# Kernel optimization log

Measured on AMD Instinct MI355X. Metric: run time of the kernel, lower is better.

The kernel has to match this reference:

```python
import jax, jax.numpy as jnp
import numpy as np

B, C, H, W = 32, 1024, 32, 32  # NOTE: code requires C == H*W (see bmm below)
C_HALF = C // 2


def setup_inputs() -> dict:
    key = jax.random.key(0)
    ks = jax.random.split(key, 7)
    s_in = 1.0 / np.sqrt(C)
    return {
        "x": jax.random.normal(ks[0], (B, C, H, W), dtype=jnp.float32),
        "Wq": jax.random.normal(ks[1], (C_HALF, C), dtype=jnp.float32) * s_in,
        "bq": jax.random.normal(ks[2], (C_HALF,), dtype=jnp.float32) * 0.01,
        "Wk": jax.random.normal(ks[3], (C_HALF, C), dtype=jnp.float32) * s_in,
        "bk": jax.random.normal(ks[4], (C_HALF,), dtype=jnp.float32) * 0.01,
        "Wv": jax.random.normal(ks[5], (C, C), dtype=jnp.float32) * s_in,
        "bv": jax.random.normal(ks[6], (C,), dtype=jnp.float32) * 0.01,
    }


def reference(x, Wq, bq, Wk, bk, Wv, bv):
    b, c, h, w = x.shape
    hw = h * w
    xf = x.reshape(b, c, hw)  # [B, C, HW]
    # 1x1 convs are per-pixel linear maps over channels
    q = jnp.einsum('oc,bcn->bno', Wq, xf) + bq            # [B, HW, C/2]  (permuted)
    k = jnp.einsum('oc,bcn->bon', Wk, xf) + bk[:, None]   # [B, C/2, HW]
    v = jnp.einsum('oc,bcn->bno', Wv, xf) + bv            # [B, HW, C]   (permuted)
    attn = jax.nn.softmax(jnp.einsum('bno,bom->bnm', q, k), axis=-1)  # [B, HW, HW]
    # torch: bmm(value [B,HW,C], attention^T [B,HW,HW]) -> requires C == HW
    out = jnp.einsum('bik,bjk->bij', v, attn)  # [B, HW(=C), HW]
    out = out.reshape(b, c, h, w)
    return out + x
```

## Files before the change

### kernel.cpp

```cpp
#include <hip/hip_runtime.h>

typedef _Float16 f16;
typedef _Float16 f16x8 __attribute__((ext_vector_type(8)));
typedef float f32x4 __attribute__((ext_vector_type(4)));

__device__ __forceinline__ void g2lds16(const void* g, void* l) {
    __builtin_amdgcn_global_load_lds(
        (const __attribute__((address_space(1))) void*)g,
        (__attribute__((address_space(3))) void*)l, 16, 0, 0);
}

__global__ __launch_bounds__(256)
void prep_w(const float* __restrict__ Wq, const float* __restrict__ bq,
            const float* __restrict__ Wk, const float* __restrict__ bk,
            const float* __restrict__ Wv, const float* __restrict__ bv,
            f16* __restrict__ Wall, float* __restrict__ ball)
{
    const int idx = blockIdx.x * 256 + threadIdx.x;
    const int o = idx >> 10;
    const int c = idx & 1023;
    float w;
    if (o < 512)        w = Wq[idx];
    else if (o < 1024)  w = Wk[idx - 512 * 1024];
    else                w = Wv[idx - 1024 * 1024];
    Wall[idx] = (f16)w;
    if (c == 0)
        ball[o] = (o < 512) ? bq[o] : (o < 1024) ? bk[o - 512] : bv[o - 1024];
}

__global__ __launch_bounds__(256)
void transpose_cast(const float* __restrict__ x, f16* __restrict__ xT)
{
    __shared__ float t[32][33];
    const int b  = blockIdx.z;
    const int c0 = blockIdx.y << 5;
    const int n0 = blockIdx.x << 5;
    const int tx = threadIdx.x & 31, ty = threadIdx.x >> 5;
    const float* xb = x + (unsigned long long)b * (1024ull * 1024ull);
#pragma unroll
    for (int i = 0; i < 32; i += 8)
        t[ty + i][tx] = xb[(unsigned long long)(c0 + ty + i) * 1024ull + (n0 + tx)];
    __syncthreads();
    f16* ob = xT + (unsigned long long)b * (1024ull * 1024ull);
#pragma unroll
    for (int i = 0; i < 32; i += 8)
        ob[(unsigned long long)(n0 + ty + i) * 1024ull + (c0 + tx)] = (f16)t[tx][ty + i];
}

template <int EPI, int LDA, int LDB, int K, int LDO,
          long long SA, long long SB, long long SO, int SWZ>
__global__ __launch_bounds__(256)
void gemm_nt(const f16* __restrict__ A, const f16* __restrict__ Bm,
             const float* __restrict__ bias,
             f16* __restrict__ Oh, float* __restrict__ Of,
             const float* __restrict__ Xres)
{
    __shared__ f16 As[2 * 128 * 32];
    __shared__ f16 Bs[2 * 128 * 32];

    const int tid  = threadIdx.x;
    const int wave = tid >> 6;
    const int lane = tid & 63;
    const int quad = lane >> 4;
    const int l16  = lane & 15;
    const int wr   = (wave >> 1) << 6;
    const int wc   = (wave & 1) << 6;

    int bm, bn;
    if (SWZ) {
        const int g = blockIdx.x >> 7;
        const int r = blockIdx.x & 127;
        bm = ((g << 3) | (r & 7)) << 7;
        bn = (r >> 3) << 7;
    } else {
        bm = blockIdx.x << 7;
        bn = blockIdx.y << 7;
    }
    const int bz = blockIdx.z;

    const f16* Ab = A  + (unsigned long long)bz * (unsigned long long)SA;
    const f16* Bb = Bm + (unsigned long long)bz * (unsigned long long)SB;

    const int srow = lane >> 2;
    const int scol = (lane & 3) << 3;

    f32x4 acc[4][4] = {};

    for (int k0 = 0; k0 < K; k0 += 64) {
        __syncthreads();
#pragma unroll
        for (int kk = 0; kk < 2; ++kk) {
#pragma unroll
            for (int t = 0; t < 2; ++t) {
                const int rbase = t * 64 + wave * 16;
                g2lds16(Ab + (unsigned long long)(bm + rbase + srow) * LDA + (k0 + kk * 32 + scol),
                        As + kk * 4096 + rbase * 32 + lane * 8);
                g2lds16(Bb + (unsigned long long)(bn + rbase + srow) * LDB + (k0 + kk * 32 + scol),
                        Bs + kk * 4096 + rbase * 32 + lane * 8);
            }
        }
        __syncthreads();

#pragma unroll
        for (int kk = 0; kk < 2; ++kk) {
            f16x8 af[4], bf[4];
#pragma unroll
            for (int i = 0; i < 4; ++i)
                af[i] = *(const f16x8*)(As + kk * 4096 + (wr + i * 16 + l16) * 32 + quad * 8);
#pragma unroll
            for (int i = 0; i < 4; ++i)
                bf[i] = *(const f16x8*)(Bs + kk * 4096 + (wc + i * 16 + l16) * 32 + quad * 8);

#pragma unroll
            for (int mi = 0; mi < 4; ++mi)
#pragma unroll
                for (int ni = 0; ni < 4; ++ni)
                    acc[mi][ni] = __builtin_amdgcn_mfma_f32_16x16x32_f16(
                        af[mi], bf[ni], acc[mi][ni], 0, 0, 0);
        }
    }

#pragma unroll
    for (int mi = 0; mi < 4; ++mi) {
#pragma unroll
        for (int v = 0; v < 4; ++v) {
            const int row = bm + wr + mi * 16 + quad * 4 + v;
#pragma unroll
            for (int ni = 0; ni < 4; ++ni) {
                const int col = bn + wc + ni * 16 + l16;
                float val = acc[mi][ni][v];
                if (EPI == 0) {
                    val += bias[col];
                    Oh[(unsigned long long)row * LDO + col] = (f16)val;
                } else if (EPI == 1) {
                    Of[(unsigned long long)bz * (unsigned long long)SO +
                       (unsigned long long)row * LDO + col] = val;
                } else {
                    const unsigned long long off =
                        (unsigned long long)bz * (unsigned long long)SO +
                        (unsigned long long)row * LDO + col;
                    Of[off] = val + Xres[off];
                }
            }
        }
    }
}

__global__ __launch_bounds__(256)
void softmax_rows(const float* __restrict__ S, f16* __restrict__ P)
{
    const unsigned long long row = blockIdx.x;
    const int tid = threadIdx.x;
    const float4 v = ((const float4*)(S + row * 1024ull))[tid];

    float m = fmaxf(fmaxf(v.x, v.y), fmaxf(v.z, v.w));
#pragma unroll
    for (int off = 32; off; off >>= 1)
        m = fmaxf(m, __shfl_xor(m, off, 64));

    __shared__ float redm[4], reds[4];
    const int wave = tid >> 6, lane = tid & 63;
    if (lane == 0) redm[wave] = m;
    __syncthreads();
    m = fmaxf(fmaxf(redm[0], redm[1]), fmaxf(redm[2], redm[3]));

    const float e0 = __expf(v.x - m), e1 = __expf(v.y - m);
    const float e2 = __expf(v.z - m), e3 = __expf(v.w - m);
    float sum = e0 + e1 + e2 + e3;
#pragma unroll
    for (int off = 32; off; off >>= 1)
        sum += __shfl_xor(sum, off, 64);
    if (lane == 0) reds[wave] = sum;
    __syncthreads();
    sum = reds[0] + reds[1] + reds[2] + reds[3];
    const float inv = 1.0f / sum;

    union { f16 h[4]; uint2 u; } pk;
    pk.h[0] = (f16)(e0 * inv); pk.h[1] = (f16)(e1 * inv);
    pk.h[2] = (f16)(e2 * inv); pk.h[3] = (f16)(e3 * inv);
    ((uint2*)(P + row * 1024ull))[tid] = pk.u;
}

extern "C" void kernel_launch(void* const* d_in, const int* in_sizes, int n_in,
                              void* d_out, int out_size, void* d_ws, size_t ws_size,
                              hipStream_t stream)
{
    const float* x  = (const float*)d_in[0];
    const float* Wq = (const float*)d_in[1];
    const float* bq = (const float*)d_in[2];
    const float* Wk = (const float*)d_in[3];
    const float* bk = (const float*)d_in[4];
    const float* Wv = (const float*)d_in[5];
    const float* bv = (const float*)d_in[6];
    float* out = (float*)d_out;

    f16*   xT   = (f16*)d_ws;
    f16*   Wall = xT + 32ull * 1024 * 1024;
    float* ball = (float*)(Wall + 2048ull * 1024);
    f16*   QKV  = (f16*)(ball + 2048);
    float* S    = (float*)(QKV + 64ull * 1024 * 1024);
    f16*   P    = (f16*)(S + 32ull * 1024 * 1024);

    prep_w<<<8192, 256, 0, stream>>>(Wq, bq, Wk, bk, Wv, bv, Wall, ball);
    transpose_cast<<<dim3(32, 32, 32), 256, 0, stream>>>(x, xT);

    gemm_nt<0, 1024, 1024, 1024, 2048, 0ll, 0ll, 0ll, 1>
        <<<dim3(4096, 1, 1), 256, 0, stream>>>(
        xT, Wall, ball, QKV, nullptr, nullptr);

    gemm_nt<1, 2048, 2048, 512, 1024, 1024ll * 2048, 1024ll * 2048, 1024ll * 1024, 0>
        <<<dim3(8, 8, 32), 256, 0, stream>>>(
        QKV, QKV + 512, nullptr, nullptr, S, nullptr);

    softmax_rows<<<32768, 256, 0, stream>>>(S, P);

    gemm_nt<2, 2048, 1024, 1024, 1024, 1024ll * 2048, 1024ll * 1024, 1024ll * 1024, 0>
        <<<dim3(8, 8, 32), 256, 0, stream>>>(
        QKV + 1024, P, nullptr, nullptr, out, x);
}
```

Before: 644.4 us.

## Switch GEMMs to 32x32x16 MFMA with XOR-swizzled LDS, XCD-aware tile mapping, vectorized transpose

The GEMM kernel now uses 32x32x16 MFMA instructions on a 2x2 accumulator tile per wave, and the LDS tile holds a single 64-wide K slab with XOR swizzling. This is meant to cut LDS bank conflicts and the number of LDS reads per MFMA. The QKV projection's block swizzle now groups tiles by XCD (blockIdx & 7) to improve L2 locality across chiplets. The transpose-cast kernel moves to 64x64 tiles with float4 loads and 8-wide f16 stores to widen memory transactions. The epilogue writes become strided per lane, and the new row mapping and swizzle carry correctness risk.

```diff
diff --git a/kernel.cpp b/kernel.cpp
--- a/kernel.cpp
+++ b/kernel.cpp
@@ -2,7 +2,7 @@
 
 typedef _Float16 f16;
 typedef _Float16 f16x8 __attribute__((ext_vector_type(8)));
-typedef float f32x4 __attribute__((ext_vector_type(4)));
+typedef float f32x16 __attribute__((ext_vector_type(16)));
 
 __device__ __forceinline__ void g2lds16(const void* g, void* l) {
     __builtin_amdgcn_global_load_lds(
@@ -31,20 +31,36 @@
 __global__ __launch_bounds__(256)
 void transpose_cast(const float* __restrict__ x, f16* __restrict__ xT)
 {
-    __shared__ float t[32][33];
+    __shared__ float t[64][65];
     const int b  = blockIdx.z;
-    const int c0 = blockIdx.y << 5;
-    const int n0 = blockIdx.x << 5;
-    const int tx = threadIdx.x & 31, ty = threadIdx.x >> 5;
+    const int c0 = blockIdx.y << 6;
+    const int n0 = blockIdx.x << 6;
+    const int tid = threadIdx.x;
     const float* xb = x + (unsigned long long)b * (1024ull * 1024ull);
-#pragma unroll
-    for (int i = 0; i < 32; i += 8)
-        t[ty + i][tx] = xb[(unsigned long long)(c0 + ty + i) * 1024ull + (n0 + tx)];
+
+    {
+        const int cl = tid >> 4;
+        const int n4 = (tid & 15) << 2;
+#pragma unroll
+        for (int i = 0; i < 64; i += 16) {
+            const float4 v = *(const float4*)(xb + (unsigned long long)(c0 + cl + i) * 1024ull + (n0 + n4));
+            t[cl + i][n4 + 0] = v.x; t[cl + i][n4 + 1] = v.y;
+            t[cl + i][n4 + 2] = v.z; t[cl + i][n4 + 3] = v.w;
+        }
+    }
     __syncthreads();
-    f16* ob = xT + (unsigned long long)b * (1024ull * 1024ull);
-#pragma unroll
-    for (int i = 0; i < 32; i += 8)
-        ob[(unsigned long long)(n0 + ty + i) * 1024ull + (c0 + tx)] = (f16)t[tx][ty + i];
+    {
+        f16* ob = xT + (unsigned long long)b * (1024ull * 1024ull);
+        const int nl = tid >> 3;
+        const int c8 = (tid & 7) << 3;
+#pragma unroll
+        for (int i = 0; i < 64; i += 32) {
+            f16x8 h;
+#pragma unroll
+            for (int j = 0; j < 8; ++j) h[j] = (f16)t[c8 + j][nl + i];
+            *(f16x8*)(ob + (unsigned long long)(n0 + nl + i) * 1024ull + (c0 + c8)) = h;
+        }
+    }
 }
 
 template <int EPI, int LDA, int LDB, int K, int LDO,
@@ -55,23 +71,28 @@
              f16* __restrict__ Oh, float* __restrict__ Of,
              const float* __restrict__ Xres)
 {
-    __shared__ f16 As[2 * 128 * 32];
-    __shared__ f16 Bs[2 * 128 * 32];
+    __shared__ f16 As[128 * 64];
+    __shared__ f16 Bs[128 * 64];
 
     const int tid  = threadIdx.x;
     const int wave = tid >> 6;
     const int lane = tid & 63;
-    const int quad = lane >> 4;
-    const int l16  = lane & 15;
+    const int l31  = lane & 31;
+    const int half = lane >> 5;
     const int wr   = (wave >> 1) << 6;
     const int wc   = (wave & 1) << 6;
 
     int bm, bn;
     if (SWZ) {
-        const int g = blockIdx.x >> 7;
-        const int r = blockIdx.x & 127;
-        bm = ((g << 3) | (r & 7)) << 7;
-        bn = (r >> 3) << 7;
+        const int xcd   = blockIdx.x & 7;
+        const int local = blockIdx.x >> 3;
+        const int stl   = local >> 6;
+        const int sub   = local & 63;
+        const int st    = stl * 8 + xcd;
+        const int bmg   = st >> 1;
+        const int bng   = st & 1;
+        bm = (bmg * 8 + (sub & 7)) << 7;
+        bn = (bng * 8 + (sub >> 3)) << 7;
     } else {
         bm = blockIdx.x << 7;
         bn = blockIdx.y << 7;
@@ -81,57 +102,56 @@
     const f16* Ab = A  + (unsigned long long)bz * (unsigned long long)SA;
     const f16* Bb = Bm + (unsigned long long)bz * (unsigned long long)SB;
 
-    const int srow = lane >> 2;
-    const int scol = (lane & 3) << 3;
-
-    f32x4 acc[4][4] = {};
+    const int srow = lane >> 3;
+    const int scol = (((lane & 7) ^ srow) << 3);
+
+    f32x16 acc[2][2] = {};
 
     for (int k0 = 0; k0 < K; k0 += 64) {
         __syncthreads();
 #pragma unroll
-        for (int kk = 0; kk < 2; ++kk) {
-#pragma unroll
-            for (int t = 0; t < 2; ++t) {
-                const int rbase = t * 64 + wave * 16;
-                g2lds16(Ab + (unsigned long long)(bm + rbase + srow) * LDA + (k0 + kk * 32 + scol),
-                        As + kk * 4096 + rbase * 32 + lane * 8);
-                g2lds16(Bb + (unsigned long long)(bn + rbase + srow) * LDB + (k0 + kk * 32 + scol),
-                        Bs + kk * 4096 + rbase * 32 + lane * 8);
+        for (int t = 0; t < 4; ++t) {
+            const int rb = t * 32 + wave * 8;
+            g2lds16(Ab + (unsigned long long)(bm + rb + srow) * LDA + (k0 + scol),
+                    As + rb * 64 + lane * 8);
+            g2lds16(Bb + (unsigned long long)(bn + rb + srow) * LDB + (k0 + scol),
+                    Bs + rb * 64 + lane * 8);
+        }
+        __syncthreads();
+
+#pragma unroll
+        for (int ks = 0; ks < 4; ++ks) {
+            const int kg = ks * 2 + half;
+            f16x8 af[2], bf[2];
+#pragma unroll
+            for (int i = 0; i < 2; ++i) {
+                const int ra = wr + i * 32 + l31;
+                af[i] = *(const f16x8*)(As + ra * 64 + ((kg ^ (ra & 7)) << 3));
+                const int rbn = wc + i * 32 + l31;
+                bf[i] = *(const f16x8*)(Bs + rbn * 64 + ((kg ^ (rbn & 7)) << 3));
             }
-        }
-        __syncthreads();
-
-#pragma unroll
-        for (int kk = 0; kk < 2; ++kk) {
-            f16x8 af[4], bf[4];
-#pragma unroll
-            for (int i = 0; i < 4; ++i)
-                af[i] = *(const f16x8*)(As + kk * 4096 + (wr + i * 16 + l16) * 32 + quad * 8);
-#pragma unroll
-            for (int i = 0; i < 4; ++i)
-                bf[i] = *(const f16x8*)(Bs + kk * 4096 + (wc + i * 16 + l16) * 32 + quad * 8);
-
-#pragma unroll
-            for (int mi = 0; mi < 4; ++mi)
-#pragma unroll
-                for (int ni = 0; ni < 4; ++ni)
-                    acc[mi][ni] = __builtin_amdgcn_mfma_f32_16x16x32_f16(
+#pragma unroll
+            for (int mi = 0; mi < 2; ++mi)
+#pragma unroll
+                for (int ni = 0; ni < 2; ++ni)
+                    acc[mi][ni] = __builtin_amdgcn_mfma_f32_32x32x16_f16(
                         af[mi], bf[ni], acc[mi][ni], 0, 0, 0);
         }
     }
 
 #pragma unroll
-    for (int mi = 0; mi < 4; ++mi) {
-#pragma unroll
-        for (int v = 0; v < 4; ++v) {
-            const int row = bm + wr + mi * 16 + quad * 4 + v;
-#pragma unroll
-            for (int ni = 0; ni < 4; ++ni) {
-                const int col = bn + wc + ni * 16 + l16;
-                float val = acc[mi][ni][v];
+    for (int mi = 0; mi < 2; ++mi) {
+#pragma unroll
+        for (int ni = 0; ni < 2; ++ni) {
+            const int col = bn + wc + ni * 32 + l31;
+            float bc = 0.0f;
+            if (EPI == 0) bc = bias[col];
+#pragma unroll
+            for (int r = 0; r < 16; ++r) {
+                const int row = bm + wr + mi * 32 + (r & 3) + 8 * (r >> 2) + 4 * half;
+                const float val = acc[mi][ni][r];
                 if (EPI == 0) {
-                    val += bias[col];
-                    Oh[(unsigned long long)row * LDO + col] = (f16)val;
+                    Oh[(unsigned long long)row * LDO + col] = (f16)(val + bc);
                 } else if (EPI == 1) {
                     Of[(unsigned long long)bz * (unsigned long long)SO +
                        (unsigned long long)row * LDO + col] = val;
@@ -202,7 +222,7 @@
     f16*   P    = (f16*)(S + 32ull * 1024 * 1024);
 
     prep_w<<<8192, 256, 0, stream>>>(Wq, bq, Wk, bk, Wv, bv, Wall, ball);
-    transpose_cast<<<dim3(32, 32, 32), 256, 0, stream>>>(x, xT);
+    transpose_cast<<<dim3(16, 16, 32), 256, 0, stream>>>(x, xT);
 
     gemm_nt<0, 1024, 1024, 1024, 2048, 0ll, 0ll, 0ll, 1>
         <<<dim3(4096, 1, 1), 256, 0, stream>>>(
```

New measurement: 628.2 us. -2.5%, faster.
